# Optimization experiments

Hardware: AMD Instinct MI355X
Metric: run time of the kernel (lower is better)

The kernel has to match this reference:

```python
import jax, jax.numpy as jnp
import numpy as np

N_NODES = 50000
D_IN = 128
D_OUT = 128
N_EDGES = 800000


def setup_inputs() -> dict:
    key = jax.random.key(0)
    ks = jax.random.split(key, 6)
    x = jax.random.normal(ks[0], (N_NODES, D_IN), dtype=jnp.float32)
    # xavier-uniform-ish init for the per-support weights
    limit = float(np.sqrt(6.0 / (D_IN + D_OUT)))
    weights = jax.random.uniform(ks[1], (2, D_IN, D_OUT), dtype=jnp.float32,
                                 minval=-limit, maxval=limit)
    edge_idx0 = jax.random.randint(ks[2], (2, N_EDGES), 0, N_NODES, dtype=jnp.int64 if jax.config.jax_enable_x64 else jnp.int32)
    vals0 = jax.random.uniform(ks[3], (N_EDGES,), dtype=jnp.float32)
    edge_idx1 = jax.random.randint(ks[4], (2, N_EDGES), 0, N_NODES, dtype=jnp.int64 if jax.config.jax_enable_x64 else jnp.int32)
    vals1 = jax.random.uniform(ks[5], (N_EDGES,), dtype=jnp.float32)
    return {"x": x, "weights": weights, "edge_idx0": edge_idx0, "vals0": vals0,
            "edge_idx1": edge_idx1, "vals1": vals1}


def _spmm(edge_idx, vals, dense, n_rows):
    # (sparse COO A) @ dense : out[row] += vals * dense[col]
    rows, cols = edge_idx[0], edge_idx[1]
    gathered = dense[cols] * vals[:, None]  # [E, D_OUT]
    return jax.ops.segment_sum(gathered, rows, num_segments=n_rows)


def reference(x, weights, edge_idx0, vals0, edge_idx1, vals1):
    n = x.shape[0]
    out = jnp.zeros((n, D_OUT), dtype=x.dtype)
    for w, ei, v in ((weights[0], edge_idx0, vals0), (weights[1], edge_idx1, vals1)):
        pre_sup = x @ w                       # [N, D_OUT] dense GEMM
        out = out + _spmm(ei, v, pre_sup, n)  # SpMM accumulate
    return jax.nn.relu(out)
```

## Files before the change

### kernel.cpp

```cpp
#include <hip/hip_runtime.h>

#define N_NODES 50000
#define D 128
#define N_EDGES 800000
#define SCAN_BLOCKS ((N_NODES + 255) / 256)
#define GEMM_BLOCKS ((N_NODES + 63) / 64)
#define BINS 196
#define NB1 256
#define CH1 3125

typedef __attribute__((ext_vector_type(8))) short short8;
typedef __attribute__((ext_vector_type(4))) float f32x4;

__device__ __forceinline__ unsigned short f2bf(float f) {
    unsigned u = __builtin_bit_cast(unsigned, f);
    u += 0x7FFFu + ((u >> 16) & 1u);
    return (unsigned short)(u >> 16);
}
__device__ __forceinline__ float bflo(unsigned p) {
    return __builtin_bit_cast(float, p << 16);
}
__device__ __forceinline__ float bfhi(unsigned p) {
    return __builtin_bit_cast(float, p & 0xFFFF0000u);
}

__global__ __launch_bounds__(256) void wt_build(const float* __restrict__ w,
                                                unsigned short* __restrict__ wt) {
    int i = blockIdx.x * 256 + threadIdx.x;
    if (i < 2 * D * D) {
        int s = i >> 14, rem = i & 16383, c = rem >> 7, k = rem & 127;
        wt[i] = f2bf(w[s * D * D + k * D + c]);
    }
}

template<int NS>
__device__ __forceinline__ void gemm_body(const float* __restrict__ x,
                                          const unsigned short* __restrict__ wt,
                                          unsigned short* __restrict__ pre0,
                                          unsigned short* __restrict__ pre1,
                                          int n_rows, int blk) {
    const int lane = threadIdx.x & 63;
    const int wid  = threadIdx.x >> 6;
    const int q    = lane >> 4;
    const int rlo  = lane & 15;
    const int r0   = blk * 64 + wid * 16;
    if (r0 >= n_rows) return;

    const float4* x4 = (const float4*)x;
    int arow  = r0 + rlo;
    int arowc = arow < n_rows ? arow : n_rows - 1;

    short8 afr[4];
    #pragma unroll
    for (int kb = 0; kb < 4; ++kb) {
        float4 fa = x4[(size_t)arowc * 32 + kb * 8 + q * 2];
        float4 fb = x4[(size_t)arowc * 32 + kb * 8 + q * 2 + 1];
        short8 a;
        a[0] = (short)f2bf(fa.x); a[1] = (short)f2bf(fa.y);
        a[2] = (short)f2bf(fa.z); a[3] = (short)f2bf(fa.w);
        a[4] = (short)f2bf(fb.x); a[5] = (short)f2bf(fb.y);
        a[6] = (short)f2bf(fb.z); a[7] = (short)f2bf(fb.w);
        afr[kb] = a;
    }

    const short8* wt8 = (const short8*)wt;
    f32x4 acc[NS][8];
    #pragma unroll
    for (int s = 0; s < NS; ++s)
        #pragma unroll
        for (int t = 0; t < 8; ++t)
            acc[s][t] = (f32x4){0.f, 0.f, 0.f, 0.f};

    #pragma unroll
    for (int t = 0; t < 8; ++t) {
        int c = t * 16 + rlo;
        #pragma unroll
        for (int kb = 0; kb < 4; ++kb) {
            short8 b0 = wt8[(size_t)c * 16 + kb * 4 + q];
            acc[0][t] = __builtin_amdgcn_mfma_f32_16x16x32_bf16(afr[kb], b0, acc[0][t], 0, 0, 0);
            if (NS == 2) {
                short8 b1 = wt8[(size_t)(D + c) * 16 + kb * 4 + q];
                acc[1][t] = __builtin_amdgcn_mfma_f32_16x16x32_bf16(afr[kb], b1, acc[1][t], 0, 0, 0);
            }
        }
    }

    #pragma unroll
    for (int i = 0; i < 4; ++i) {
        int rw = r0 + q * 4 + i;
        if (rw < n_rows) {
            #pragma unroll
            for (int t = 0; t < 8; ++t) {
                pre0[(size_t)rw * D + t * 16 + rlo] = f2bf(acc[0][t][i]);
                if (NS == 2) pre1[(size_t)rw * D + t * 16 + rlo] = f2bf(acc[1][t][i]);
            }
        }
    }
}


__global__ __launch_bounds__(256) void p1_count(const int* __restrict__ r0,
                                                const int* __restrict__ r1,
                                                int* __restrict__ h) {
    int s = blockIdx.y, blk = blockIdx.x;
    const int* r = s ? r1 : r0;
    __shared__ int hist[BINS];
    for (int i = threadIdx.x; i < BINS; i += 256) hist[i] = 0;
    __syncthreads();
    int start = blk * CH1, end = start + CH1;
    for (int e = start + (int)threadIdx.x; e < end; e += 256)
        atomicAdd(&hist[r[e] >> 8], 1);
    __syncthreads();
    for (int i = threadIdx.x; i < BINS; i += 256)
        h[(size_t)(s * NB1 + blk) * BINS + i] = hist[i];
}

__global__ __launch_bounds__(256) void binred(const int* __restrict__ h,
                                              int* __restrict__ bintot) {
    int s = blockIdx.y, bin = blockIdx.x, t = threadIdx.x;
    int v = h[(size_t)(s * NB1 + t) * BINS + bin];
    const int lane = t & 63, wid = t >> 6;
    __shared__ int ws[4];
    #pragma unroll
    for (int o = 32; o > 0; o >>= 1) v += __shfl_down(v, o);
    if (lane == 0) ws[wid] = v;
    __syncthreads();
    if (t == 0) bintot[s * BINS + bin] = ws[0] + ws[1] + ws[2] + ws[3];
}

__global__ __launch_bounds__(256) void binscan(const int* __restrict__ bintot,
                                               int* __restrict__ binbase) {
    int s = blockIdx.x, t = threadIdx.x;
    int v = (t < BINS) ? bintot[s * BINS + t] : 0;
    const int lane = t & 63, wid = t >> 6;
    __shared__ int ws[4];
    int incl = v;
    #pragma unroll
    for (int o = 1; o < 64; o <<= 1) { int tv = __shfl_up(incl, o); if (lane >= o) incl += tv; }
    if (lane == 63) ws[wid] = incl;
    __syncthreads();
    int wbase = 0;
    #pragma unroll
    for (int j = 0; j < 4; ++j) wbase += (j < wid) ? ws[j] : 0;
    int excl = wbase + incl - v;
    if (t < BINS) binbase[s * (BINS + 1) + t] = excl;
    if (t == BINS - 1) binbase[s * (BINS + 1) + BINS] = excl + v;
}

__global__ __launch_bounds__(256) void blkscan(int* __restrict__ h,
                                               const int* __restrict__ binbase) {
    int s = blockIdx.y, bin = blockIdx.x, t = threadIdx.x;
    size_t idx = (size_t)(s * NB1 + t) * BINS + bin;
    int v = h[idx];
    const int lane = t & 63, wid = t >> 6;
    __shared__ int ws[4];
    int incl = v;
    #pragma unroll
    for (int o = 1; o < 64; o <<= 1) { int tv = __shfl_up(incl, o); if (lane >= o) incl += tv; }
    if (lane == 63) ws[wid] = incl;
    __syncthreads();
    int wbase = 0;
    #pragma unroll
    for (int j = 0; j < 4; ++j) wbase += (j < wid) ? ws[j] : 0;
    h[idx] = binbase[s * (BINS + 1) + bin] + (wbase + incl - v);
}

__global__ __launch_bounds__(256) void k_fill_gemm(const float* __restrict__ x,
                                                   const unsigned short* __restrict__ wt,
                                                   unsigned short* __restrict__ pre0,
                                                   unsigned short* __restrict__ pre1,
                                                   const int* __restrict__ r0, const int* __restrict__ c0,
                                                   const float* __restrict__ v0,
                                                   const int* __restrict__ r1, const int* __restrict__ c1,
                                                   const float* __restrict__ v1,
                                                   const int* __restrict__ h,
                                                   int2* __restrict__ rec, int n_rows) {
    int bid = blockIdx.x;
    if (bid < 2 * NB1) {
        int s = bid & 1, blk = bid >> 1;
        const int*   r = s ? r1 : r0;
        const int*   c = s ? c1 : c0;
        const float* v = s ? v1 : v0;
        int2* rs = rec + (size_t)s * N_EDGES;
        __shared__ int base[BINS];
        __shared__ int cnt2[BINS];
        for (int i = threadIdx.x; i < BINS; i += 256) {
            base[i] = h[(size_t)(s * NB1 + blk) * BINS + i];
            cnt2[i] = 0;
        }
        __syncthreads();
        int start = blk * CH1, end = start + CH1;
        for (int e = start + (int)threadIdx.x; e < end; e += 256) {
            int rr = r[e], cc = c[e];
            float vv = v[e];
            int bin = rr >> 8;
            int lr = atomicAdd(&cnt2[bin], 1);
            rs[base[bin] + lr] = make_int2((cc << 8) | (rr & 255), __float_as_int(vv));
        }
    } else {
        gemm_body<2>(x, wt, pre0, pre1, n_rows, bid - 2 * NB1);
    }
}

__global__ __launch_bounds__(512) void p2_sort(const int* __restrict__ binbase,
                                               const int2* __restrict__ rec,
                                               int2* __restrict__ ep,
                                               int* __restrict__ off) {
    int s = blockIdx.y, bin = blockIdx.x, t = threadIdx.x;
    int bs  = binbase[s * (BINS + 1) + bin];
    int be  = binbase[s * (BINS + 1) + bin + 1];
    int cnt = be - bs;
    const int2* rs = rec + (size_t)s * N_EDGES;
    int2* es = ep + (size_t)s * N_EDGES;
    __shared__ int lc[256];
    __shared__ int cur[256];
    __shared__ int ws[4];
    if (t < 256) lc[t] = 0;
    __syncthreads();
    for (int i = t; i < cnt; i += 512)
        atomicAdd(&lc[rs[bs + i].x & 255], 1);
    __syncthreads();
    const int lane = t & 63, wid = t >> 6;
    int v = 0, incl = 0;
    if (t < 256) {
        v = lc[t];
        incl = v;
        #pragma unroll
        for (int o = 1; o < 64; o <<= 1) { int tv = __shfl_up(incl, o); if (lane >= o) incl += tv; }
        if (lane == 63) ws[wid] = incl;
    }
    __syncthreads();
    if (t < 256) {
        int wbase = 0;
        #pragma unroll
        for (int j = 0; j < 4; ++j) wbase += (j < wid) ? ws[j] : 0;
        int excl = wbase + incl - v;
        int row = bin * 256 + t;
        if (row < N_NODES) off[s * (N_NODES + 1) + row] = bs + excl;
        cur[t] = excl;
    }
    if (bin == 0 && t == 0) off[s * (N_NODES + 1) + N_NODES] = N_EDGES;
    __syncthreads();
    for (int i = t; i < cnt; i += 512) {
        int2 R = rs[bs + i];
        int p = atomicAdd(&cur[R.x & 255], 1);
        es[bs + p] = make_int2(R.x >> 8, R.y);
    }
}

__device__ __forceinline__ void row_acc(const int2* __restrict__ ep,
                                        const unsigned short* __restrict__ pre,
                                        int b, int e, int lane, float& ax, float& ay) {
    int i = b;
    for (; i + 7 < e; i += 8) {
        int2 E[8];
        unsigned P[8];
        #pragma unroll
        for (int j = 0; j < 8; ++j) E[j] = ep[i + j];
        #pragma unroll
        for (int j = 0; j < 8; ++j) P[j] = *(const unsigned*)(pre + (size_t)E[j].x * D + 2 * lane);
        #pragma unroll
        for (int j = 0; j < 8; ++j) {
            float w = __int_as_float(E[j].y);
            ax = fmaf(w, bflo(P[j]), ax);
            ay = fmaf(w, bfhi(P[j]), ay);
        }
    }
    if (i + 3 < e) {
        int2 E[4];
        unsigned P[4];
        #pragma unroll
        for (int j = 0; j < 4; ++j) E[j] = ep[i + j];
        #pragma unroll
        for (int j = 0; j < 4; ++j) P[j] = *(const unsigned*)(pre + (size_t)E[j].x * D + 2 * lane);
        #pragma unroll
        for (int j = 0; j < 4; ++j) {
            float w = __int_as_float(E[j].y);
            ax = fmaf(w, bflo(P[j]), ax);
            ay = fmaf(w, bfhi(P[j]), ay);
        }
        i += 4;
    }
    for (; i < e; ++i) {
        int2 e0 = ep[i];
        float w = __int_as_float(e0.y);
        unsigned p = *(const unsigned*)(pre + (size_t)e0.x * D + 2 * lane);
        ax = fmaf(w, bflo(p), ax);
        ay = fmaf(w, bfhi(p), ay);
    }
}

__global__ __launch_bounds__(256) void gather_fused(const int* __restrict__ off_base,
                                                    const int2* __restrict__ ep_base,
                                                    const unsigned short* __restrict__ pre0,
                                                    const unsigned short* __restrict__ pre1,
                                                    float* __restrict__ out, int n_rows) {
    const int lane = threadIdx.x & 63;
    const int wid  = threadIdx.x >> 6;
    const int wpg  = 4 * gridDim.x;
    const int2* ep1b = ep_base + N_EDGES;
    const int* o1 = off_base + (N_NODES + 1);
    float2* out2 = (float2*)out;
    for (int r = blockIdx.x * 4 + wid; r < n_rows; r += wpg) {
        float ax0 = 0.f, ay0 = 0.f, ax1 = 0.f, ay1 = 0.f;
        int i0 = off_base[r], e0 = off_base[r + 1];
        int i1 = o1[r],       e1 = o1[r + 1];
        while (i0 + 7 < e0 && i1 + 7 < e1) {
            int2 E0[8], E1[8];
            unsigned P0[8], P1[8];
            #pragma unroll
            for (int j = 0; j < 8; ++j) { E0[j] = ep_base[i0 + j]; E1[j] = ep1b[i1 + j]; }
            #pragma unroll
            for (int j = 0; j < 8; ++j) {
                P0[j] = *(const unsigned*)(pre0 + (size_t)E0[j].x * D + 2 * lane);
                P1[j] = *(const unsigned*)(pre1 + (size_t)E1[j].x * D + 2 * lane);
            }
            #pragma unroll
            for (int j = 0; j < 8; ++j) {
                float w0 = __int_as_float(E0[j].y);
                float w1 = __int_as_float(E1[j].y);
                ax0 = fmaf(w0, bflo(P0[j]), ax0);
                ay0 = fmaf(w0, bfhi(P0[j]), ay0);
                ax1 = fmaf(w1, bflo(P1[j]), ax1);
                ay1 = fmaf(w1, bfhi(P1[j]), ay1);
            }
            i0 += 8; i1 += 8;
        }
        row_acc(ep_base, pre0, i0, e0, lane, ax0, ay0);
        row_acc(ep1b,    pre1, i1, e1, lane, ax1, ay1);
        float2 o;
        o.x = fmaxf(ax0 + ax1, 0.f);
        o.y = fmaxf(ay0 + ay1, 0.f);
        out2[(size_t)r * 64 + lane] = o;
    }
}

__global__ __launch_bounds__(256) void gemm_mfma2(const float* __restrict__ x,
                                                  const unsigned short* __restrict__ wt,
                                                  unsigned short* __restrict__ pre0,
                                                  unsigned short* __restrict__ pre1, int n_rows) {
    gemm_body<2>(x, wt, pre0, pre1, n_rows, blockIdx.x);
}
__global__ __launch_bounds__(256) void gemm_mfma1(const float* __restrict__ x,
                                                  const unsigned short* __restrict__ wt,
                                                  unsigned short* __restrict__ pre, int n_rows) {
    gemm_body<1>(x, wt, pre, pre, n_rows, blockIdx.x);
}

__global__ __launch_bounds__(256) void hist_rank(const int* __restrict__ r0,
                                                 const int* __restrict__ r1,
                                                 int* __restrict__ cnt_base,
                                                 int* __restrict__ rank_base, int n_edges) {
    int s = blockIdx.y;
    const int* r = s ? r1 : r0;
    int* cnt  = cnt_base + s * N_NODES;
    int* rank = rank_base + (size_t)s * N_EDGES;
    for (int e = blockIdx.x * 256 + threadIdx.x; e < n_edges; e += gridDim.x * 256)
        rank[e] = atomicAdd(&cnt[r[e]], 1);
}

__global__ __launch_bounds__(256) void scanA(const int* __restrict__ cnt_base,
                                             int* __restrict__ bsum) {
    int s = blockIdx.y;
    int i = blockIdx.x * 256 + threadIdx.x;
    int v = (i < N_NODES) ? cnt_base[s * N_NODES + i] : 0;
    const int lane = threadIdx.x & 63;
    const int wid  = threadIdx.x >> 6;
    __shared__ int ws[4];
    #pragma unroll
    for (int off = 32; off > 0; off >>= 1) v += __shfl_down(v, off);
    if (lane == 0) ws[wid] = v;
    __syncthreads();
    if (threadIdx.x == 0)
        bsum[s * SCAN_BLOCKS + blockIdx.x] = ws[0] + ws[1] + ws[2] + ws[3];
}

__global__ __launch_bounds__(256) void scanC2(const int* __restrict__ cnt_base,
                                              const int* __restrict__ bsum,
                                              int* __restrict__ off_base) {
    int s = blockIdx.y;
    int t = threadIdx.x;
    const int lane = t & 63;
    const int wid  = t >> 6;
    __shared__ int ws[4];
    __shared__ int base_s;
    int bv = (t < (int)blockIdx.x && t < SCAN_BLOCKS) ? bsum[s * SCAN_BLOCKS + t] : 0;
    #pragma unroll
    for (int off = 32; off > 0; off >>= 1) bv += __shfl_down(bv, off);
    if (lane == 0) ws[wid] = bv;
    __syncthreads();
    if (t == 0) base_s = ws[0] + ws[1] + ws[2] + ws[3];
    __syncthreads();
    int base = base_s;
    __syncthreads();
    int i = blockIdx.x * 256 + t;
    int v = (i < N_NODES) ? cnt_base[s * N_NODES + i] : 0;
    int incl = v;
    #pragma unroll
    for (int off = 1; off < 64; off <<= 1) {
        int tv = __shfl_up(incl, off);
        if (lane >= off) incl += tv;
    }
    if (lane == 63) ws[wid] = incl;
    __syncthreads();
    int wbase = 0;
    #pragma unroll
    for (int j = 0; j < 4; ++j) wbase += (j < wid) ? ws[j] : 0;
    int* off = off_base + s * (N_NODES + 1);
    if (i < N_NODES)
        off[i] = base + wbase + incl - v;
    if (blockIdx.x == 0 && t == 0)
        off[N_NODES] = N_EDGES;
}

__global__ __launch_bounds__(256) void scatter_csr(const int* __restrict__ r0, const int* __restrict__ c0,
                                                   const float* __restrict__ v0,
                                                   const int* __restrict__ r1, const int* __restrict__ c1,
                                                   const float* __restrict__ v1,
                                                   const int* __restrict__ off_base,
                                                   const int* __restrict__ rank_base,
                                                   int2* __restrict__ ep_base, int n_edges) {
    int s = blockIdx.y;
    const int*   r    = s ? r1 : r0;
    const int*   c    = s ? c1 : c0;
    const float* v    = s ? v1 : v0;
    const int*   off  = off_base + s * (N_NODES + 1);
    const int*   rank = rank_base + (size_t)s * N_EDGES;
    int2* ep = ep_base + (size_t)s * N_EDGES;
    for (int e = blockIdx.x * 256 + threadIdx.x; e < n_edges; e += gridDim.x * 256) {
        int p = off[r[e]] + rank[e];
        int2 rec;
        rec.x = c[e];
        rec.y = __float_as_int(v[e]);
        ep[p] = rec;
    }
}

template<int ACCUM_RELU>
__global__ __launch_bounds__(256) void gather_one(const int* __restrict__ off,
                                                  const int2* __restrict__ ep,
                                                  const unsigned short* __restrict__ pre,
                                                  float* __restrict__ out, int n_rows) {
    const int lane = threadIdx.x & 63;
    const int wid  = threadIdx.x >> 6;
    const int wpg  = 4 * gridDim.x;
    float2* out2 = (float2*)out;
    for (int r = blockIdx.x * 4 + wid; r < n_rows; r += wpg) {
        float ax = 0.f, ay = 0.f;
        row_acc(ep, pre, off[r], off[r + 1], lane, ax, ay);
        float2 o;
        if (ACCUM_RELU) {
            float2 prev = out2[(size_t)r * 64 + lane];
            o.x = fmaxf(prev.x + ax, 0.f);
            o.y = fmaxf(prev.y + ay, 0.f);
        } else {
            o.x = ax; o.y = ay;
        }
        out2[(size_t)r * 64 + lane] = o;
    }
}

extern "C" void kernel_launch(void* const* d_in, const int* in_sizes, int n_in,
                              void* d_out, int out_size, void* d_ws, size_t ws_size,
                              hipStream_t stream) {
    const float* x       = (const float*)d_in[0];
    const float* weights = (const float*)d_in[1];
    const int*   ei0     = (const int*)d_in[2];
    const float* v0      = (const float*)d_in[3];
    const int*   ei1     = (const int*)d_in[4];
    const float* v1      = (const float*)d_in[5];
    float* out = (float*)d_out;

    dim3 blk(256);
    const size_t PRE_B = (size_t)N_NODES * D * sizeof(unsigned short);
    const size_t WT_B  = (size_t)2 * D * D * sizeof(unsigned short);
    const size_t H_B   = (size_t)2 * NB1 * BINS * 4;
    const size_t BT_B  = (size_t)2 * BINS * 4;
    const size_t BB_B  = (size_t)2 * (BINS + 1) * 4;
    const size_t OFF_B = (size_t)2 * (N_NODES + 1) * 4;
    const size_t E8    = (size_t)2 * N_EDGES * sizeof(int2);

    char* wsb = (char*)d_ws;
    size_t needNew = 2 * PRE_B + WT_B + H_B + BT_B + BB_B + OFF_B + 2 * E8;
    size_t needA1 = 2 * PRE_B + WT_B
                  + (size_t)(2 * (N_NODES + 1) + 2 * N_NODES + 2 * SCAN_BLOCKS) * 4
                  + E8 + (size_t)2 * N_EDGES * 4;

    if (ws_size >= needNew) {
        unsigned short* pre0 = (unsigned short*)wsb;
        unsigned short* pre1 = (unsigned short*)(wsb + PRE_B);
        unsigned short* wt   = (unsigned short*)(wsb + 2 * PRE_B);
        int*  h       = (int*)(wsb + 2 * PRE_B + WT_B);
        int*  bintot  = (int*)((char*)h + H_B);
        int*  binbase = (int*)((char*)bintot + BT_B);
        int*  off     = (int*)((char*)binbase + BB_B);
        int2* rec     = (int2*)((char*)off + OFF_B);
        int2* ep      = rec + (size_t)2 * N_EDGES;

        wt_build<<<128, blk, 0, stream>>>(weights, wt);
        p1_count<<<dim3(NB1, 2), blk, 0, stream>>>(ei0, ei1, h);
        binred  <<<dim3(BINS, 2), blk, 0, stream>>>(h, bintot);
        binscan <<<2, blk, 0, stream>>>(bintot, binbase);
        blkscan <<<dim3(BINS, 2), blk, 0, stream>>>(h, binbase);
        k_fill_gemm<<<2 * NB1 + GEMM_BLOCKS, blk, 0, stream>>>(
            x, wt, pre0, pre1,
            ei0, ei0 + N_EDGES, v0, ei1, ei1 + N_EDGES, v1,
            h, rec, N_NODES);
        p2_sort<<<dim3(BINS, 2), dim3(512), 0, stream>>>(binbase, rec, ep, off);
        gather_fused<<<12500, blk, 0, stream>>>(off, ep, pre0, pre1, out, N_NODES);
    } else if (ws_size >= needA1) {
        unsigned short* pre0 = (unsigned short*)wsb;
        unsigned short* pre1 = (unsigned short*)(wsb + PRE_B);
        unsigned short* wt   = (unsigned short*)(wsb + 2 * PRE_B);
        int*  off  = (int*)(wsb + 2 * PRE_B + WT_B);
        int*  cnt  = off + 2 * (N_NODES + 1);
        int*  bsum = cnt + 2 * N_NODES;
        int2* ep   = (int2*)(bsum + 2 * SCAN_BLOCKS);
        int*  rank = (int*)(ep + (size_t)2 * N_EDGES);

        hipMemsetAsync(cnt, 0, (size_t)2 * N_NODES * sizeof(int), stream);
        wt_build<<<128, blk, 0, stream>>>(weights, wt);
        hist_rank<<<dim3(1024, 2), blk, 0, stream>>>(ei0, ei1, cnt, rank, N_EDGES);
        gemm_mfma2<<<GEMM_BLOCKS, blk, 0, stream>>>(x, wt, pre0, pre1, N_NODES);
        scanA<<<dim3(SCAN_BLOCKS, 2), blk, 0, stream>>>(cnt, bsum);
        scanC2<<<dim3(SCAN_BLOCKS, 2), blk, 0, stream>>>(cnt, bsum, off);
        scatter_csr<<<dim3(1024, 2), blk, 0, stream>>>(ei0, ei0 + N_EDGES, v0,
                                                       ei1, ei1 + N_EDGES, v1,
                                                       off, rank, ep, N_EDGES);
        gather_fused<<<12500, blk, 0, stream>>>(off, ep, pre0, pre1, out, N_NODES);
    } else {
        unsigned short* pre = (unsigned short*)wsb;
        unsigned short* wt  = (unsigned short*)(wsb + PRE_B);
        int*  off  = (int*)(wsb + PRE_B + WT_B);
        int*  cnt  = off + (N_NODES + 1);
        int*  bsum = cnt + N_NODES;
        int2* ep   = (int2*)(bsum + SCAN_BLOCKS);
        int*  rank = (int*)pre;

        wt_build<<<128, blk, 0, stream>>>(weights, wt);
        const int* rows[2] = {ei0, ei1};
        const int* cols[2] = {ei0 + N_EDGES, ei1 + N_EDGES};
        const float* vals[2] = {v0, v1};
        for (int s = 0; s < 2; ++s) {
            hipMemsetAsync(cnt, 0, (size_t)N_NODES * sizeof(int), stream);
            hist_rank<<<dim3(1024, 1), blk, 0, stream>>>(rows[s], rows[s], cnt, rank, N_EDGES);
            scanA<<<dim3(SCAN_BLOCKS, 1), blk, 0, stream>>>(cnt, bsum);
            scanC2<<<dim3(SCAN_BLOCKS, 1), blk, 0, stream>>>(cnt, bsum, off);
            scatter_csr<<<dim3(1024, 1), blk, 0, stream>>>(rows[s], cols[s], vals[s],
                                                           rows[s], cols[s], vals[s],
                                                           off, rank, ep, N_EDGES);
            gemm_mfma1<<<GEMM_BLOCKS, blk, 0, stream>>>(x, wt + (size_t)s * D * D, pre, N_NODES);
            if (s == 0)
                gather_one<0><<<12500, blk, 0, stream>>>(off, ep, pre, out, N_NODES);
            else
                gather_one<1><<<12500, blk, 0, stream>>>(off, ep, pre, out, N_NODES);
        }
    }
}
```

Baseline: 144.5 us.

## Split GEMM across three sort-phase kernels and merge bin reduce with scan

The dense GEMM blocks, once all in the fill kernel, are now split into three groups. They are co-launched with the histogram count, fill and per-bin sort kernels, so the bandwidth-light sort phases overlap with MFMA work. The separate bin-reduction and bin-scan kernels are merged into one two-block kernel that serially sums the per-block histograms. The sort kernel also moves from 512 to 256 threads per block to match the GEMM block shape. This removes two launches and idle gaps at the cost of a slower serial reduction and uneven block mixes.

```diff
diff --git a/kernel.cpp b/kernel.cpp
--- a/kernel.cpp
+++ b/kernel.cpp
@@ -8,6 +8,12 @@
 #define BINS 196
 #define NB1 256
 #define CH1 3125
+#define G1 250
+#define G1_OFF 0
+#define G2 282
+#define G2_OFF 250
+#define G3 250
+#define G3_OFF 532
 
 typedef __attribute__((ext_vector_type(8))) short short8;
 typedef __attribute__((ext_vector_type(4))) float f32x4;
@@ -99,39 +105,43 @@
 }
 
 
-__global__ __launch_bounds__(256) void p1_count(const int* __restrict__ r0,
-                                                const int* __restrict__ r1,
-                                                int* __restrict__ h) {
-    int s = blockIdx.y, blk = blockIdx.x;
-    const int* r = s ? r1 : r0;
-    __shared__ int hist[BINS];
-    for (int i = threadIdx.x; i < BINS; i += 256) hist[i] = 0;
-    __syncthreads();
-    int start = blk * CH1, end = start + CH1;
-    for (int e = start + (int)threadIdx.x; e < end; e += 256)
-        atomicAdd(&hist[r[e] >> 8], 1);
-    __syncthreads();
-    for (int i = threadIdx.x; i < BINS; i += 256)
-        h[(size_t)(s * NB1 + blk) * BINS + i] = hist[i];
-}
-
-__global__ __launch_bounds__(256) void binred(const int* __restrict__ h,
-                                              int* __restrict__ bintot) {
-    int s = blockIdx.y, bin = blockIdx.x, t = threadIdx.x;
-    int v = h[(size_t)(s * NB1 + t) * BINS + bin];
-    const int lane = t & 63, wid = t >> 6;
-    __shared__ int ws[4];
-    #pragma unroll
-    for (int o = 32; o > 0; o >>= 1) v += __shfl_down(v, o);
-    if (lane == 0) ws[wid] = v;
-    __syncthreads();
-    if (t == 0) bintot[s * BINS + bin] = ws[0] + ws[1] + ws[2] + ws[3];
-}
-
-__global__ __launch_bounds__(256) void binscan(const int* __restrict__ bintot,
-                                               int* __restrict__ binbase) {
+__global__ __launch_bounds__(256) void k_p1_gemm(const float* __restrict__ x,
+                                                 const unsigned short* __restrict__ wt,
+                                                 unsigned short* __restrict__ pre0,
+                                                 unsigned short* __restrict__ pre1,
+                                                 const int* __restrict__ r0,
+                                                 const int* __restrict__ r1,
+                                                 int* __restrict__ h, int n_rows) {
+    int bid = blockIdx.x;
+    if (bid < 2 * NB1) {
+        int s = bid & 1, blk = bid >> 1;
+        const int* r = s ? r1 : r0;
+        __shared__ int hist[BINS];
+        for (int i = threadIdx.x; i < BINS; i += 256) hist[i] = 0;
+        __syncthreads();
+        int start = blk * CH1, end = start + CH1;
+        for (int e = start + (int)threadIdx.x; e < end; e += 256)
+            atomicAdd(&hist[r[e] >> 8], 1);
+        __syncthreads();
+        for (int i = threadIdx.x; i < BINS; i += 256)
+            h[(size_t)(s * NB1 + blk) * BINS + i] = hist[i];
+    } else {
+        gemm_body<2>(x, wt, pre0, pre1, n_rows, bid - 2 * NB1 + G1_OFF);
+    }
+}
+
+__global__ __launch_bounds__(256) void binredscan(const int* __restrict__ h,
+                                                  int* __restrict__ binbase) {
     int s = blockIdx.x, t = threadIdx.x;
-    int v = (t < BINS) ? bintot[s * BINS + t] : 0;
+    int acc[8] = {0, 0, 0, 0, 0, 0, 0, 0};
+    if (t < BINS) {
+        for (int blk = 0; blk < NB1; blk += 8) {
+            #pragma unroll
+            for (int j = 0; j < 8; ++j)
+                acc[j] += h[(size_t)(s * NB1 + blk + j) * BINS + t];
+        }
+    }
+    int v = acc[0] + acc[1] + acc[2] + acc[3] + acc[4] + acc[5] + acc[6] + acc[7];
     const int lane = t & 63, wid = t >> 6;
     __shared__ int ws[4];
     int incl = v;
@@ -198,53 +208,58 @@
             rs[base[bin] + lr] = make_int2((cc << 8) | (rr & 255), __float_as_int(vv));
         }
     } else {
-        gemm_body<2>(x, wt, pre0, pre1, n_rows, bid - 2 * NB1);
-    }
-}
-
-__global__ __launch_bounds__(512) void p2_sort(const int* __restrict__ binbase,
-                                               const int2* __restrict__ rec,
-                                               int2* __restrict__ ep,
-                                               int* __restrict__ off) {
-    int s = blockIdx.y, bin = blockIdx.x, t = threadIdx.x;
-    int bs  = binbase[s * (BINS + 1) + bin];
-    int be  = binbase[s * (BINS + 1) + bin + 1];
-    int cnt = be - bs;
-    const int2* rs = rec + (size_t)s * N_EDGES;
-    int2* es = ep + (size_t)s * N_EDGES;
-    __shared__ int lc[256];
-    __shared__ int cur[256];
-    __shared__ int ws[4];
-    if (t < 256) lc[t] = 0;
-    __syncthreads();
-    for (int i = t; i < cnt; i += 512)
-        atomicAdd(&lc[rs[bs + i].x & 255], 1);
-    __syncthreads();
-    const int lane = t & 63, wid = t >> 6;
-    int v = 0, incl = 0;
-    if (t < 256) {
-        v = lc[t];
-        incl = v;
+        gemm_body<2>(x, wt, pre0, pre1, n_rows, bid - 2 * NB1 + G2_OFF);
+    }
+}
+
+__global__ __launch_bounds__(256) void k_p2_gemm(const float* __restrict__ x,
+                                                 const unsigned short* __restrict__ wt,
+                                                 unsigned short* __restrict__ pre0,
+                                                 unsigned short* __restrict__ pre1,
+                                                 const int* __restrict__ binbase,
+                                                 const int2* __restrict__ rec,
+                                                 int2* __restrict__ ep,
+                                                 int* __restrict__ off, int n_rows) {
+    int bid = blockIdx.x;
+    if (bid < 2 * BINS) {
+        int s = bid & 1, bin = bid >> 1;
+        int t = threadIdx.x;
+        int bs  = binbase[s * (BINS + 1) + bin];
+        int be  = binbase[s * (BINS + 1) + bin + 1];
+        int cnt = be - bs;
+        const int2* rs = rec + (size_t)s * N_EDGES;
+        int2* es = ep + (size_t)s * N_EDGES;
+        __shared__ int lc[256];
+        __shared__ int cur[256];
+        __shared__ int ws[4];
+        lc[t] = 0;
+        __syncthreads();
+        for (int i = t; i < cnt; i += 256)
+            atomicAdd(&lc[rs[bs + i].x & 255], 1);
+        __syncthreads();
+        const int lane = t & 63, wid = t >> 6;
+        int v = lc[t];
+        int incl = v;
         #pragma unroll
         for (int o = 1; o < 64; o <<= 1) { int tv = __shfl_up(incl, o); if (lane >= o) incl += tv; }
         if (lane == 63) ws[wid] = incl;
-    }
-    __syncthreads();
-    if (t < 256) {
+        __syncthreads();
         int wbase = 0;
         #pragma unroll
         for (int j = 0; j < 4; ++j) wbase += (j < wid) ? ws[j] : 0;
         int excl = wbase + incl - v;
         int row = bin * 256 + t;
         if (row < N_NODES) off[s * (N_NODES + 1) + row] = bs + excl;
+        if (bin == 0 && t == 0) off[s * (N_NODES + 1) + N_NODES] = N_EDGES;
         cur[t] = excl;
-    }
-    if (bin == 0 && t == 0) off[s * (N_NODES + 1) + N_NODES] = N_EDGES;
-    __syncthreads();
-    for (int i = t; i < cnt; i += 512) {
-        int2 R = rs[bs + i];
-        int p = atomicAdd(&cur[R.x & 255], 1);
-        es[bs + p] = make_int2(R.x >> 8, R.y);
+        __syncthreads();
+        for (int i = t; i < cnt; i += 256) {
+            int2 R = rs[bs + i];
+            int p = atomicAdd(&cur[R.x & 255], 1);
+            es[bs + p] = make_int2(R.x >> 8, R.y);
+        }
+    } else {
+        gemm_body<2>(x, wt, pre0, pre1, n_rows, bid - 2 * BINS + G3_OFF);
     }
 }
 
@@ -475,13 +490,12 @@
     const size_t PRE_B = (size_t)N_NODES * D * sizeof(unsigned short);
     const size_t WT_B  = (size_t)2 * D * D * sizeof(unsigned short);
     const size_t H_B   = (size_t)2 * NB1 * BINS * 4;
-    const size_t BT_B  = (size_t)2 * BINS * 4;
     const size_t BB_B  = (size_t)2 * (BINS + 1) * 4;
     const size_t OFF_B = (size_t)2 * (N_NODES + 1) * 4;
     const size_t E8    = (size_t)2 * N_EDGES * sizeof(int2);
 
     char* wsb = (char*)d_ws;
-    size_t needNew = 2 * PRE_B + WT_B + H_B + BT_B + BB_B + OFF_B + 2 * E8;
+    size_t needNew = 2 * PRE_B + WT_B + H_B + BB_B + OFF_B + 2 * E8;
     size_t needA1 = 2 * PRE_B + WT_B
                   + (size_t)(2 * (N_NODES + 1) + 2 * N_NODES + 2 * SCAN_BLOCKS) * 4
                   + E8 + (size_t)2 * N_EDGES * 4;
@@ -491,22 +505,21 @@
         unsigned short* pre1 = (unsigned short*)(wsb + PRE_B);
         unsigned short* wt   = (unsigned short*)(wsb + 2 * PRE_B);
         int*  h       = (int*)(wsb + 2 * PRE_B + WT_B);
-        int*  bintot  = (int*)((char*)h + H_B);
-        int*  binbase = (int*)((char*)bintot + BT_B);
+        int*  binbase = (int*)((char*)h + H_B);
         int*  off     = (int*)((char*)binbase + BB_B);
         int2* rec     = (int2*)((char*)off + OFF_B);
         int2* ep      = rec + (size_t)2 * N_EDGES;
 
         wt_build<<<128, blk, 0, stream>>>(weights, wt);
-        p1_count<<<dim3(NB1, 2), blk, 0, stream>>>(ei0, ei1, h);
-        binred  <<<dim3(BINS, 2), blk, 0, stream>>>(h, bintot);
-        binscan <<<2, blk, 0, stream>>>(bintot, binbase);
-        blkscan <<<dim3(BINS, 2), blk, 0, stream>>>(h, binbase);
-        k_fill_gemm<<<2 * NB1 + GEMM_BLOCKS, blk, 0, stream>>>(
+        k_p1_gemm<<<2 * NB1 + G1, blk, 0, stream>>>(x, wt, pre0, pre1, ei0, ei1, h, N_NODES);
+        binredscan<<<2, blk, 0, stream>>>(h, binbase);
+        blkscan<<<dim3(BINS, 2), blk, 0, stream>>>(h, binbase);
+        k_fill_gemm<<<2 * NB1 + G2, blk, 0, stream>>>(
             x, wt, pre0, pre1,
             ei0, ei0 + N_EDGES, v0, ei1, ei1 + N_EDGES, v1,
             h, rec, N_NODES);
-        p2_sort<<<dim3(BINS, 2), dim3(512), 0, stream>>>(binbase, rec, ep, off);
+        k_p2_gemm<<<2 * BINS + G3, blk, 0, stream>>>(x, wt, pre0, pre1,
+                                                     binbase, rec, ep, off, N_NODES);
         gather_fused<<<12500, blk, 0, stream>>>(off, ep, pre0, pre1, out, N_NODES);
     } else if (ws_size >= needA1) {
         unsigned short* pre0 = (unsigned short*)wsb;
```

New measurement: 153.9 us. 6.6% more time.

## Pack edge records into 32-bit col+bf16 weight and sub-sort by column

Applied to the files above, without the earlier changes.

The CSR sort now emits 4-byte edge records holding a 16-bit column and a bf16 weight, instead of 8-byte int2 records. It also refines the within-bin sort key with the column's high bits, so each row's edges are grouped by column range. A new gather kernel decodes the packed records. This halves edge-stream traffic in both the sort output and the gather, at the cost of bf16 precision on edge weights and a larger shared-memory histogram.

```diff
diff --git a/kernel.cpp b/kernel.cpp
--- a/kernel.cpp
+++ b/kernel.cpp
@@ -8,6 +8,7 @@
 #define BINS 196
 #define NB1 256
 #define CH1 3125
+#define NKEY 2048
 
 typedef __attribute__((ext_vector_type(8))) short short8;
 typedef __attribute__((ext_vector_type(4))) float f32x4;
@@ -204,47 +205,142 @@
 
 __global__ __launch_bounds__(512) void p2_sort(const int* __restrict__ binbase,
                                                const int2* __restrict__ rec,
-                                               int2* __restrict__ ep,
+                                               unsigned* __restrict__ ep,
                                                int* __restrict__ off) {
     int s = blockIdx.y, bin = blockIdx.x, t = threadIdx.x;
     int bs  = binbase[s * (BINS + 1) + bin];
     int be  = binbase[s * (BINS + 1) + bin + 1];
     int cnt = be - bs;
     const int2* rs = rec + (size_t)s * N_EDGES;
-    int2* es = ep + (size_t)s * N_EDGES;
-    __shared__ int lc[256];
-    __shared__ int cur[256];
-    __shared__ int ws[4];
-    if (t < 256) lc[t] = 0;
-    __syncthreads();
-    for (int i = t; i < cnt; i += 512)
-        atomicAdd(&lc[rs[bs + i].x & 255], 1);
-    __syncthreads();
-    const int lane = t & 63, wid = t >> 6;
-    int v = 0, incl = 0;
-    if (t < 256) {
-        v = lc[t];
-        incl = v;
-        #pragma unroll
-        for (int o = 1; o < 64; o <<= 1) { int tv = __shfl_up(incl, o); if (lane >= o) incl += tv; }
-        if (lane == 63) ws[wid] = incl;
-    }
-    __syncthreads();
-    if (t < 256) {
-        int wbase = 0;
-        #pragma unroll
-        for (int j = 0; j < 4; ++j) wbase += (j < wid) ? ws[j] : 0;
-        int excl = wbase + incl - v;
-        int row = bin * 256 + t;
-        if (row < N_NODES) off[s * (N_NODES + 1) + row] = bs + excl;
-        cur[t] = excl;
-    }
-    if (bin == 0 && t == 0) off[s * (N_NODES + 1) + N_NODES] = N_EDGES;
+    unsigned* es = ep + (size_t)s * N_EDGES;
+    __shared__ int lc[NKEY];
+    __shared__ int cur[NKEY];
+    __shared__ int ws[8];
+    #pragma unroll
+    for (int j = 0; j < NKEY / 512; ++j) lc[t + j * 512] = 0;
     __syncthreads();
     for (int i = t; i < cnt; i += 512) {
         int2 R = rs[bs + i];
-        int p = atomicAdd(&cur[R.x & 255], 1);
-        es[bs + p] = make_int2(R.x >> 8, R.y);
+        int col = R.x >> 8;
+        int key = ((R.x & 255) << 3) | (col >> 13);
+        atomicAdd(&lc[key], 1);
+    }
+    __syncthreads();
+    int kb = t * 4;
+    int s0 = lc[kb], s1 = lc[kb + 1], s2 = lc[kb + 2], s3 = lc[kb + 3];
+    int tot = s0 + s1 + s2 + s3;
+    const int lane = t & 63, wid = t >> 6;
+    int incl = tot;
+    #pragma unroll
+    for (int o = 1; o < 64; o <<= 1) { int tv = __shfl_up(incl, o); if (lane >= o) incl += tv; }
+    if (lane == 63) ws[wid] = incl;
+    __syncthreads();
+    int wbase = 0;
+    #pragma unroll
+    for (int j = 0; j < 8; ++j) wbase += (j < wid) ? ws[j] : 0;
+    int excl = wbase + incl - tot;
+    cur[kb]     = excl;
+    cur[kb + 1] = excl + s0;
+    cur[kb + 2] = excl + s0 + s1;
+    cur[kb + 3] = excl + s0 + s1 + s2;
+    if ((t & 1) == 0) {
+        int row = bin * 256 + (t >> 1);
+        if (row < N_NODES) off[s * (N_NODES + 1) + row] = bs + excl;
+    }
+    if (bin == 0 && t == 0) off[s * (N_NODES + 1) + N_NODES] = N_EDGES;
+    __syncthreads();
+    for (int i = t; i < cnt; i += 512) {
+        int2 R = rs[bs + i];
+        int col = R.x >> 8;
+        int key = ((R.x & 255) << 3) | (col >> 13);
+        int p = atomicAdd(&cur[key], 1);
+        es[bs + p] = ((unsigned)col << 16) | (unsigned)f2bf(__int_as_float(R.y));
+    }
+}
+
+__device__ __forceinline__ void row_acc4(const unsigned* __restrict__ ep,
+                                         const unsigned* __restrict__ prew,
+                                         int b, int e, int lane, float& ax, float& ay) {
+    int i = b;
+    for (; i + 7 < e; i += 8) {
+        unsigned E[8], P[8];
+        #pragma unroll
+        for (int j = 0; j < 8; ++j) E[j] = ep[i + j];
+        #pragma unroll
+        for (int j = 0; j < 8; ++j) P[j] = prew[(size_t)(E[j] >> 16) * 64 + lane];
+        #pragma unroll
+        for (int j = 0; j < 8; ++j) {
+            float w = bflo(E[j]);
+            ax = fmaf(w, bflo(P[j]), ax);
+            ay = fmaf(w, bfhi(P[j]), ay);
+        }
+    }
+    if (i + 3 < e) {
+        unsigned E[4], P[4];
+        #pragma unroll
+        for (int j = 0; j < 4; ++j) E[j] = ep[i + j];
+        #pragma unroll
+        for (int j = 0; j < 4; ++j) P[j] = prew[(size_t)(E[j] >> 16) * 64 + lane];
+        #pragma unroll
+        for (int j = 0; j < 4; ++j) {
+            float w = bflo(E[j]);
+            ax = fmaf(w, bflo(P[j]), ax);
+            ay = fmaf(w, bfhi(P[j]), ay);
+        }
+        i += 4;
+    }
+    for (; i < e; ++i) {
+        unsigned E = ep[i];
+        float w = bflo(E);
+        unsigned p = prew[(size_t)(E >> 16) * 64 + lane];
+        ax = fmaf(w, bflo(p), ax);
+        ay = fmaf(w, bfhi(p), ay);
+    }
+}
+
+__global__ __launch_bounds__(256) void gather_fused4(const int* __restrict__ off_base,
+                                                     const unsigned* __restrict__ ep_base,
+                                                     const unsigned short* __restrict__ pre0,
+                                                     const unsigned short* __restrict__ pre1,
+                                                     float* __restrict__ out, int n_rows) {
+    const int lane = threadIdx.x & 63;
+    const int wid  = threadIdx.x >> 6;
+    const int wpg  = 4 * gridDim.x;
+    const unsigned* ep1b = ep_base + N_EDGES;
+    const int* o1 = off_base + (N_NODES + 1);
+    const unsigned* pre0w = (const unsigned*)pre0;
+    const unsigned* pre1w = (const unsigned*)pre1;
+    float2* out2 = (float2*)out;
+    for (int r = blockIdx.x * 4 + wid; r < n_rows; r += wpg) {
+        float ax0 = 0.f, ay0 = 0.f, ax1 = 0.f, ay1 = 0.f;
+        int i0 = off_base[r], e0 = off_base[r + 1];
+        int i1 = o1[r],       e1 = o1[r + 1];
+        while (i0 + 7 < e0 && i1 + 7 < e1) {
+            unsigned E0[8], E1[8], P0[8], P1[8];
+            #pragma unroll
+            for (int j = 0; j < 8; ++j) { E0[j] = ep_base[i0 + j]; E1[j] = ep1b[i1 + j]; }
+            #pragma unroll
+            for (int j = 0; j < 8; ++j) {
+                P0[j] = pre0w[(size_t)(E0[j] >> 16) * 64 + lane];
+                P1[j] = pre1w[(size_t)(E1[j] >> 16) * 64 + lane];
+            }
+            #pragma unroll
+            for (int j = 0; j < 8; ++j) {
+                float w0 = bflo(E0[j]);
+                float w1 = bflo(E1[j]);
+                ax0 = fmaf(w0, bflo(P0[j]), ax0);
+                ay0 = fmaf(w0, bfhi(P0[j]), ay0);
+                ax1 = fmaf(w1, bflo(P1[j]), ax1);
+                ay1 = fmaf(w1, bfhi(P1[j]), ay1);
+            }
+            i0 += 8; i1 += 8;
+        }
+        row_acc4(ep_base, pre0w, i0, e0, lane, ax0, ay0);
+        row_acc4(ep1b,    pre1w, i1, e1, lane, ax1, ay1);
+        float2 o;
+        o.x = fmaxf(ax0 + ax1, 0.f);
+        o.y = fmaxf(ay0 + ay1, 0.f);
+        out2[(size_t)r * 64 + lane] = o;
     }
 }
 
@@ -265,21 +361,6 @@
             ax = fmaf(w, bflo(P[j]), ax);
             ay = fmaf(w, bfhi(P[j]), ay);
         }
-    }
-    if (i + 3 < e) {
-        int2 E[4];
-        unsigned P[4];
-        #pragma unroll
-        for (int j = 0; j < 4; ++j) E[j] = ep[i + j];
-        #pragma unroll
-        for (int j = 0; j < 4; ++j) P[j] = *(const unsigned*)(pre + (size_t)E[j].x * D + 2 * lane);
-        #pragma unroll
-        for (int j = 0; j < 4; ++j) {
-            float w = __int_as_float(E[j].y);
-            ax = fmaf(w, bflo(P[j]), ax);
-            ay = fmaf(w, bfhi(P[j]), ay);
-        }
-        i += 4;
     }
     for (; i < e; ++i) {
         int2 e0 = ep[i];
@@ -303,31 +384,8 @@
     float2* out2 = (float2*)out;
     for (int r = blockIdx.x * 4 + wid; r < n_rows; r += wpg) {
         float ax0 = 0.f, ay0 = 0.f, ax1 = 0.f, ay1 = 0.f;
-        int i0 = off_base[r], e0 = off_base[r + 1];
-        int i1 = o1[r],       e1 = o1[r + 1];
-        while (i0 + 7 < e0 && i1 + 7 < e1) {
-            int2 E0[8], E1[8];
-            unsigned P0[8], P1[8];
-            #pragma unroll
-            for (int j = 0; j < 8; ++j) { E0[j] = ep_base[i0 + j]; E1[j] = ep1b[i1 + j]; }
-            #pragma unroll
-            for (int j = 0; j < 8; ++j) {
-                P0[j] = *(const unsigned*)(pre0 + (size_t)E0[j].x * D + 2 * lane);
-                P1[j] = *(const unsigned*)(pre1 + (size_t)E1[j].x * D + 2 * lane);
-            }
-            #pragma unroll
-            for (int j = 0; j < 8; ++j) {
-                float w0 = __int_as_float(E0[j].y);
-                float w1 = __int_as_float(E1[j].y);
-                ax0 = fmaf(w0, bflo(P0[j]), ax0);
-                ay0 = fmaf(w0, bfhi(P0[j]), ay0);
-                ax1 = fmaf(w1, bflo(P1[j]), ax1);
-                ay1 = fmaf(w1, bfhi(P1[j]), ay1);
-            }
-            i0 += 8; i1 += 8;
-        }
-        row_acc(ep_base, pre0, i0, e0, lane, ax0, ay0);
-        row_acc(ep1b,    pre1, i1, e1, lane, ax1, ay1);
+        row_acc(ep_base, pre0, off_base[r], off_base[r + 1], lane, ax0, ay0);
+        row_acc(ep1b,    pre1, o1[r], o1[r + 1], lane, ax1, ay1);
         float2 o;
         o.x = fmaxf(ax0 + ax1, 0.f);
         o.y = fmaxf(ay0 + ay1, 0.f);
@@ -479,9 +537,10 @@
     const size_t BB_B  = (size_t)2 * (BINS + 1) * 4;
     const size_t OFF_B = (size_t)2 * (N_NODES + 1) * 4;
     const size_t E8    = (size_t)2 * N_EDGES * sizeof(int2);
+    const size_t E4    = (size_t)2 * N_EDGES * 4;
 
     char* wsb = (char*)d_ws;
-    size_t needNew = 2 * PRE_B + WT_B + H_B + BT_B + BB_B + OFF_B + 2 * E8;
+    size_t needNew = 2 * PRE_B + WT_B + H_B + BT_B + BB_B + OFF_B + E8 + E4;
     size_t needA1 = 2 * PRE_B + WT_B
                   + (size_t)(2 * (N_NODES + 1) + 2 * N_NODES + 2 * SCAN_BLOCKS) * 4
                   + E8 + (size_t)2 * N_EDGES * 4;
@@ -495,7 +554,7 @@
         int*  binbase = (int*)((char*)bintot + BT_B);
         int*  off     = (int*)((char*)binbase + BB_B);
         int2* rec     = (int2*)((char*)off + OFF_B);
-        int2* ep      = rec + (size_t)2 * N_EDGES;
+        unsigned* ep  = (unsigned*)(rec + (size_t)2 * N_EDGES);
 
         wt_build<<<128, blk, 0, stream>>>(weights, wt);
         p1_count<<<dim3(NB1, 2), blk, 0, stream>>>(ei0, ei1, h);
@@ -507,7 +566,7 @@
             ei0, ei0 + N_EDGES, v0, ei1, ei1 + N_EDGES, v1,
             h, rec, N_NODES);
         p2_sort<<<dim3(BINS, 2), dim3(512), 0, stream>>>(binbase, rec, ep, off);
-        gather_fused<<<12500, blk, 0, stream>>>(off, ep, pre0, pre1, out, N_NODES);
+        gather_fused4<<<12500, blk, 0, stream>>>(off, ep, pre0, pre1, out, N_NODES);
     } else if (ws_size >= needA1) {
         unsigned short* pre0 = (unsigned short*)wsb;
         unsigned short* pre1 = (unsigned short*)(wsb + PRE_B);
```

After: 141.3 us. 2.2% less time.
